# Kernel optimization log

Hardware: AMD Instinct MI355X
Metric: run time of the kernel (lower is better)

## Reference

```python
import jax, jax.numpy as jnp
import numpy as np

B, N = 64, 128
SELF_DIM, AGENT_DIM = 6, 7
C = 32            # in_mlp_dims[-1] == ia_mlp_dims[-1]
GRU_H = 2 * C     # 64
DN = ('NCHW', 'OIHW', 'NCHW')


def _lin(key, out_d, in_d):
    k1, k2 = jax.random.split(key)
    s = 1.0 / np.sqrt(in_d)
    w = jax.random.uniform(k1, (out_d, in_d), minval=-s, maxval=s, dtype=jnp.float32)
    b = jax.random.uniform(k2, (out_d,), minval=-s, maxval=s, dtype=jnp.float32)
    return w, b


def setup_inputs() -> dict:
    ks = jax.random.split(jax.random.key(0), 20)
    d = {}
    d['state'] = jax.random.normal(ks[0], (B, N, SELF_DIM + AGENT_DIM), jnp.float32)
    d['w_in1'], d['b_in1'] = _lin(ks[1], 64, AGENT_DIM)
    d['w_in2'], d['b_in2'] = _lin(ks[2], C, 64)
    s1 = 1.0 / np.sqrt(C * 9)
    d['w_c1'] = jax.random.uniform(ks[3], (64, C, 3, 3), minval=-s1, maxval=s1, dtype=jnp.float32)
    d['b_c1'] = jnp.zeros((64,), jnp.float32)
    s2 = 1.0 / np.sqrt(64 * 9)
    d['w_c2'] = jax.random.uniform(ks[4], (C, 64, 3, 3), minval=-s2, maxval=s2, dtype=jnp.float32)
    d['b_c2'] = jnp.zeros((C,), jnp.float32)
    d['w_ia1'], d['b_ia1'] = _lin(ks[5], 64, C)
    d['w_ia2'], d['b_ia2'] = _lin(ks[6], C, 64)
    d['w_s1'], d['b_s1'] = _lin(ks[7], 64, C + SELF_DIM)
    d['w_s2'], d['b_s2'] = _lin(ks[8], 32, 64)
    d['w_a1'], d['b_a1'] = _lin(ks[9], 64, 64)
    d['w_a2'], d['b_a2'] = _lin(ks[10], 32, 64)
    d['w_a3'], d['b_a3'] = _lin(ks[11], 1, 32)
    d['w_z'], _ = _lin(ks[12], GRU_H, 2 * GRU_H)
    d['w_r'], _ = _lin(ks[13], GRU_H, 2 * GRU_H)
    d['w_q'], _ = _lin(ks[14], GRU_H, 2 * GRU_H)
    d['w_m1'], d['b_m1'] = _lin(ks[15], 128, GRU_H + SELF_DIM)
    d['w_m2'], d['b_m2'] = _lin(ks[16], 64, 128)
    d['w_m3'], d['b_m3'] = _lin(ks[17], 1, 64)
    return d


def _forward(state, w_in1, b_in1, w_in2, b_in2, w_c1, b_c1, w_c2, b_c2,
             w_ia1, b_ia1, w_ia2, b_ia2, w_s1, b_s1, w_s2, b_s2,
             w_a1, b_a1, w_a2, b_a2, w_a3, b_a3, w_z, w_r, w_q,
             w_m1, b_m1, w_m2, b_m2, w_m3, b_m3):
    self_state = state[:, :, :SELF_DIM]            # (B, N, 6)
    agents = state[:, :, SELF_DIM:]                # (B, N, 7)

    # input_mlp (last_relu=True)
    h = jax.nn.relu(agents @ w_in1.T + b_in1)
    in_out = jax.nn.relu(h @ w_in2.T + b_in2)      # (B, N, C)

    # ---- AFAModule: pairwise N x N construction + conv2d edge-MLP + softmax agg ----
    f = in_out.transpose(0, 2, 1)                  # (B, C, N)
    eye = jnp.eye(N, dtype=f.dtype)
    # pair[b,c,i,j] = f[b,c,i] - f[b,c,j] + f[b,c,i]*delta_ij
    pair = f[:, :, :, None] - f[:, :, None, :] + f[:, :, :, None] * eye  # (B, C, N, N)
    w = jax.lax.conv_general_dilated(pair, w_c1, (1, 1), 'SAME', dimension_numbers=DN)
    w = jax.nn.relu(w + b_c1[None, :, None, None])
    w = jax.lax.conv_general_dilated(w, w_c2, (1, 1), 'SAME', dimension_numbers=DN)
    w = w + b_c2[None, :, None, None]
    w = jax.nn.softmax(w, axis=-1)
    afa = (pair * w).sum(-1)                        # (B, C, N)
    afa = afa.reshape(B, N, C)                      # faithful to torch .view (no transpose)
    x = in_out + afa

    # ia_mlp
    h1 = jax.nn.relu(x @ w_ia1.T + b_ia1)
    ia = h1 @ w_ia2.T + b_ia2                       # (B, N, C)

    # sort_mlp
    sort_in = jnp.concatenate([ia, self_state], axis=-1)  # (B, N, C+6)
    s1 = jax.nn.relu(sort_in @ w_s1.T + b_s1)
    sort_out = s1 @ w_s2.T + b_s2                   # (B, N, 32)
    gstate = jnp.broadcast_to(jnp.mean(sort_out, 1, keepdims=True), (B, N, 32))
    sort_mlp_input = jnp.concatenate([sort_out, gstate], axis=-1)  # (B, N, 64)

    # attention scores with masked-exp normalization
    a1 = jax.nn.relu(sort_mlp_input @ w_a1.T + b_a1)
    a2 = jax.nn.relu(a1 @ w_a2.T + b_a2)
    scores = (a2 @ w_a3.T + b_a3)[..., 0]           # (B, N)
    scores_exp = jnp.exp(scores) * (scores != 0).astype(scores.dtype)
    weights = (scores_exp / jnp.sum(scores_exp, 1, keepdims=True))[..., None]
    weighted = weights * sort_mlp_input             # (B, N, 64)

    # custom conv1d GRU (kernel 1, no bias -> channel matmuls)
    gru_input = weighted.reshape(B, GRU_H, N)       # faithful to torch .view
    h0 = sort_mlp_input.transpose(0, 2, 1)          # (B, 64, N)
    hx = jnp.concatenate([h0, gru_input], axis=1)   # (B, 128, N)
    z = jax.nn.sigmoid(jnp.einsum('oc,bcn->bon', w_z, hx))
    r = jax.nn.sigmoid(jnp.einsum('oc,bcn->bon', w_r, hx))
    q = jnp.tanh(jnp.einsum('oc,bcn->bon', w_q, jnp.concatenate([r * h0, gru_input], axis=1)))
    hn = (1 - z) * h0 + z * q
    hn = jnp.mean(hn, axis=2)                       # (B, 64)

    joint = jnp.concatenate([self_state[:, 0, :], hn], axis=1)  # (B, 70)
    m1 = jax.nn.relu(joint @ w_m1.T + b_m1)
    m2 = jax.nn.relu(m1 @ w_m2.T + b_m2)
    value = m2 @ w_m3.T + b_m3
    return value.reshape(B, -1)


def reference(state, w_in1, b_in1, w_in2, b_in2, w_c1, b_c1, w_c2, b_c2,
              w_ia1, b_ia1, w_ia2, b_ia2, w_s1, b_s1, w_s2, b_s2,
              w_a1, b_a1, w_a2, b_a2, w_a3, b_a3, w_z, w_r, w_q,
              w_m1, b_m1, w_m2, b_m2, w_m3, b_m3):
    return _forward(state, w_in1, b_in1, w_in2, b_in2, w_c1, b_c1, w_c2, b_c2,
                    w_ia1, b_ia1, w_ia2, b_ia2, w_s1, b_s1, w_s2, b_s2,
                    w_a1, b_a1, w_a2, b_a2, w_a3, b_a3, w_z, w_r, w_q,
                    w_m1, b_m1, w_m2, b_m2, w_m3, b_m3)
```

## Files before the change

kernel.cpp:

```cpp
#include <hip/hip_runtime.h>
#include <math.h>


typedef short bf16x8 __attribute__((ext_vector_type(8)));
typedef float f32x16 __attribute__((ext_vector_type(16)));

__device__ inline unsigned int bf16_rne(float x) {
  unsigned int u = __float_as_uint(x);
  return (u + 0x7fffu + ((u >> 16) & 1u)) >> 16;
}

#define MF(A, B, Cc) __builtin_amdgcn_mfma_f32_32x32x16_bf16((A), (B), (Cc), 0, 0, 0)

__global__ __launch_bounds__(256) void k0_pack(const float* __restrict__ w_c2,
                                               unsigned short* __restrict__ Apack) {
  for (int idx = threadIdx.x; idx < 36864; idx += 256) {
    int p = idx / 18432, rem = idx % 18432;
    int rx = rem >> 11, r2 = rem & 2047;
    int chunk = r2 >> 9, r3 = r2 & 511;
    int lane = r3 >> 3, i8 = r3 & 7;
    int o2 = lane & 31, k8 = lane >> 5;
    int cin = chunk * 16 + k8 * 8 + i8;
    float v = w_c2[(o2 * 64 + cin) * 9 + rx];
    unsigned int hi = bf16_rne(v);
    float hif = __uint_as_float(hi << 16);
    unsigned int lo = bf16_rne(v - hif);
    Apack[idx] = (unsigned short)(p ? lo : hi);
  }
}

__global__ __launch_bounds__(128) void k1_front(
    const float* __restrict__ state, const float* __restrict__ w_in1,
    const float* __restrict__ b_in1, const float* __restrict__ w_in2,
    const float* __restrict__ b_in2, float* __restrict__ f) {
  int b = blockIdx.x, nq = blockIdx.y, t = threadIdx.x;
  int row = t >> 2, lane = t & 3;
  int n = nq * 32 + row;
  __shared__ float hs[32][66];
  const float* st = state + (b * 128 + n) * 13 + 6;
  float a[7];
#pragma unroll
  for (int k = 0; k < 7; k++) a[k] = st[k];
  for (int oi = 0; oi < 16; oi++) {
    int o = lane * 16 + oi;
    float acc = b_in1[o];
#pragma unroll
    for (int k = 0; k < 7; k++) acc += w_in1[o * 7 + k] * a[k];
    hs[row][o] = fmaxf(acc, 0.f);
  }
  __syncthreads();
  for (int ci = 0; ci < 8; ci++) {
    int c = lane * 8 + ci;
    float acc = b_in2[c];
#pragma unroll 8
    for (int k = 0; k < 64; k++) acc += w_in2[c * 64 + k] * hs[row][k];
    f[(b * 32 + c) * 128 + n] = fmaxf(acc, 0.f);
  }
}

__global__ __launch_bounds__(128) void k2_pre(
    const float* __restrict__ f, const float* __restrict__ w_c1,
    float* __restrict__ R, float* __restrict__ C, float* __restrict__ D) {
  int o = blockIdx.x, b = blockIdx.y, t = threadIdx.x;
  __shared__ float fL[32 * 128];
  __shared__ float w1s[32 * 9];
  __shared__ float wrow[32 * 9];
  __shared__ float wcol[32 * 9];
  for (int idx = t; idx < 4096; idx += 128) fL[idx] = f[b * 4096 + idx];
  for (int idx = t; idx < 288; idx += 128) w1s[idx] = w_c1[o * 288 + idx];
  __syncthreads();
  if (t < 32) {
    int c = t;
#pragma unroll
    for (int di = 0; di < 3; di++) {
      float w0 = w1s[c * 9 + di * 3 + 0], w1 = w1s[c * 9 + di * 3 + 1],
            w2 = w1s[c * 9 + di * 3 + 2];
      wrow[(c * 3 + di) * 3 + 0] = w1 + w2;
      wrow[(c * 3 + di) * 3 + 1] = w0 + w1 + w2;
      wrow[(c * 3 + di) * 3 + 2] = w0 + w1;
    }
#pragma unroll
    for (int dj = 0; dj < 3; dj++) {
      float w0 = w1s[c * 9 + 0 * 3 + dj], w1 = w1s[c * 9 + 1 * 3 + dj],
            w2 = w1s[c * 9 + 2 * 3 + dj];
      wcol[(c * 3 + dj) * 3 + 0] = w1 + w2;
      wcol[(c * 3 + dj) * 3 + 1] = w0 + w1 + w2;
      wcol[(c * 3 + dj) * 3 + 2] = w0 + w1;
    }
  }
  __syncthreads();
  int i = t;
  float r0 = 0, r1 = 0, r2 = 0, c0 = 0, c1 = 0, c2 = 0;
  float d0 = 0, d1 = 0, d2 = 0, d3 = 0, d4 = 0;
  for (int c = 0; c < 32; c++) {
    float fm = (i >= 1) ? fL[c * 128 + i - 1] : 0.f;
    float f0 = fL[c * 128 + i];
    float fp = (i < 127) ? fL[c * 128 + i + 1] : 0.f;
    const float* wr = &wrow[c * 9];
    r0 += fm * wr[0] + f0 * wr[3] + fp * wr[6];
    r1 += fm * wr[1] + f0 * wr[4] + fp * wr[7];
    r2 += fm * wr[2] + f0 * wr[5] + fp * wr[8];
    const float* wc = &wcol[c * 9];
    c0 += fm * wc[0] + f0 * wc[3] + fp * wc[6];
    c1 += fm * wc[1] + f0 * wc[4] + fp * wc[7];
    c2 += fm * wc[2] + f0 * wc[5] + fp * wc[8];
    const float* wp = &w1s[c * 9];
    d0 += fm * wp[2];
    d1 += fm * wp[1] + f0 * wp[5];
    d2 += fm * wp[0] + f0 * wp[4] + fp * wp[8];
    d3 += f0 * wp[3] + fp * wp[7];
    d4 += fp * wp[6];
  }
  R[((b * 3 + 0) * 64 + o) * 128 + i] = r0;
  R[((b * 3 + 1) * 64 + o) * 128 + i] = r1;
  R[((b * 3 + 2) * 64 + o) * 128 + i] = r2;
  C[((b * 3 + 0) * 64 + o) * 128 + i] = c0;
  C[((b * 3 + 1) * 64 + o) * 128 + i] = c1;
  C[((b * 3 + 2) * 64 + o) * 128 + i] = c2;
  float* dp = &D[((b * 64 + o) * 128 + i) * 5];
  dp[0] = d0; dp[1] = d1; dp[2] = d2; dp[3] = d3; dp[4] = d4;
}

__global__ __launch_bounds__(256, 2) void k3_conv2(
    const float* __restrict__ f, const float* __restrict__ R,
    const float* __restrict__ C, const float* __restrict__ D,
    const float* __restrict__ b_c1, const unsigned short* __restrict__ Apack,
    const float* __restrict__ b_c2, float* __restrict__ afa) {
  extern __shared__ unsigned short G[];
  int iblk = blockIdx.x, b = blockIdx.y, t = threadIdx.x;
  int i0 = iblk * 2;
  int lane = t & 63, jt = t >> 6;
  int nn = lane & 31;
  int ccoff_half = (lane >> 5) * 8;
  const bf16x8* A8 = (const bf16x8*)Apack;
  bf16x8 zero8 = {0, 0, 0, 0, 0, 0, 0, 0};
  f32x16 acc0 = {0, 0, 0, 0, 0, 0, 0, 0, 0, 0, 0, 0, 0, 0, 0, 0};
  f32x16 acc1 = {0, 0, 0, 0, 0, 0, 0, 0, 0, 0, 0, 0, 0, 0, 0, 0};

  int ccp = t >> 2;
  int ipl = ccp >> 4;
  int cpr = ccp & 15;
  int q = t & 3;
  int j0r = q * 32;
  int ip = i0 - 1 + ipl;
  bool rowok = (ip >= 0 && ip <= 127);
  int ipc = ip < 0 ? 0 : (ip > 127 ? 127 : ip);
  int ic = (ipc == 0) ? 0 : ((ipc == 127) ? 2 : 1);

  for (int half = 0; half < 2; half++) {
    if (half) __syncthreads();
    {
      int cc = half * 32 + cpr * 2;
      float bias0 = b_c1[cc], bias1 = b_c1[cc + 1];
      float base0 = R[((b * 3 + 1) * 64 + cc) * 128 + ipc] + bias0;
      float base1 = R[((b * 3 + 1) * 64 + cc + 1) * 128 + ipc] + bias1;
      float r0v0 = 0, r0v1 = 0, r2v0 = 0, r2v1 = 0;
      if (q == 0) {
        r0v0 = R[((b * 3 + 0) * 64 + cc) * 128 + ipc] + bias0;
        r0v1 = R[((b * 3 + 0) * 64 + cc + 1) * 128 + ipc] + bias1;
      }
      if (q == 3) {
        r2v0 = R[((b * 3 + 2) * 64 + cc) * 128 + ipc] + bias0;
        r2v1 = R[((b * 3 + 2) * 64 + cc + 1) * 128 + ipc] + bias1;
      }
      const float* C0 = &C[((b * 3 + ic) * 64 + cc) * 128 + j0r];
      const float* C1 = C0 + 128;
      const float* D0 = &D[((b * 64 + cc) * 128 + ipc) * 5];
      const float* D1 = D0 + 640;
      unsigned int gbase = (unsigned)((ipl * 128 + j0r) * 40 + 2 * cpr);
#pragma unroll
      for (int s4i = 0; s4i < 8; s4i++) {
        int s4 = (s4i + q) & 7;
        float4 c0 = ((const float4*)C0)[s4];
        float4 c1 = ((const float4*)C1)[s4];
        float v0[4], v1[4];
        v0[0] = base0 - c0.x; v0[1] = base0 - c0.y;
        v0[2] = base0 - c0.z; v0[3] = base0 - c0.w;
        v1[0] = base1 - c1.x; v1[1] = base1 - c1.y;
        v1[2] = base1 - c1.z; v1[3] = base1 - c1.w;
        if (q == 0 && s4 == 0) { v0[0] = r0v0 - c0.x; v1[0] = r0v1 - c1.x; }
        if (q == 3 && s4 == 7) { v0[3] = r2v0 - c0.w; v1[3] = r2v1 - c1.w; }
#pragma unroll
        for (int t5 = 0; t5 < 5; t5++) {
          int rel = (ip - 2 + t5) - (j0r + s4 * 4);
          if (rel >= 0 && rel < 4) { v0[rel] += D0[t5]; v1[rel] += D1[t5]; }
        }
#pragma unroll
        for (int k = 0; k < 4; k++) {
          float a0 = rowok ? fmaxf(v0[k], 0.f) : 0.f;
          float a1 = rowok ? fmaxf(v1[k], 0.f) : 0.f;
          unsigned int h0 = bf16_rne(a0), h1 = bf16_rne(a1);
          float l0f = a0 - __uint_as_float(h0 << 16);
          float l1f = a1 - __uint_as_float(h1 << 16);
          unsigned int l0 = bf16_rne(l0f), l1 = bf16_rne(l1f);
          unsigned int off = gbase + (unsigned)((s4 * 4 + k) * 40);
          *(unsigned int*)&G[off] = h0 | (h1 << 16);
          *(unsigned int*)&G[off + 20480] = l0 | (l1 << 16);
        }
      }
    }
    __syncthreads();
    for (int cb = 0; cb < 2; cb++) {
      int chunk = half * 2 + cb;
      bf16x8 Ah[9], Al[9];
#pragma unroll
      for (int rx = 0; rx < 9; rx++) {
        Ah[rx] = A8[(rx * 4 + chunk) * 64 + lane];
        Al[rx] = A8[((9 + rx) * 4 + chunk) * 64 + lane];
      }
      int ccoff = cb * 16 + ccoff_half;
#pragma unroll
      for (int rowidx = 0; rowidx < 4; rowidx++) {
#pragma unroll
        for (int x = 0; x < 3; x++) {
          int imgj = jt * 32 + nn + x - 1;
          int ij = imgj < 0 ? 0 : (imgj > 127 ? 127 : imgj);
          int off = (rowidx * 128 + ij) * 40 + ccoff;
          bf16x8 bh = *(const bf16x8*)&G[off];
          bf16x8 bl = *(const bf16x8*)&G[off + 20480];
          if (imgj < 0 || imgj > 127) { bh = zero8; bl = zero8; }
          if (rowidx == 0) {
            acc0 = MF(Ah[x], bh, acc0);
            acc0 = MF(Ah[x], bl, acc0);
            acc0 = MF(Al[x], bh, acc0);
          } else if (rowidx == 1) {
            acc0 = MF(Ah[3 + x], bh, acc0);
            acc0 = MF(Ah[3 + x], bl, acc0);
            acc0 = MF(Al[3 + x], bh, acc0);
            acc1 = MF(Ah[x], bh, acc1);
            acc1 = MF(Ah[x], bl, acc1);
            acc1 = MF(Al[x], bh, acc1);
          } else if (rowidx == 2) {
            acc0 = MF(Ah[6 + x], bh, acc0);
            acc0 = MF(Ah[6 + x], bl, acc0);
            acc0 = MF(Al[6 + x], bh, acc0);
            acc1 = MF(Ah[3 + x], bh, acc1);
            acc1 = MF(Ah[3 + x], bl, acc1);
            acc1 = MF(Al[3 + x], bh, acc1);
          } else {
            acc1 = MF(Ah[6 + x], bh, acc1);
            acc1 = MF(Ah[6 + x], bl, acc1);
            acc1 = MF(Al[6 + x], bh, acc1);
          }
        }
      }
    }
  }
  __syncthreads();
  const int LSTR = 129;
  float* logits = (float*)G;
  float* fbuf = (float*)G + 64 * LSTR;
#pragma unroll
  for (int reg = 0; reg < 16; reg++) {
    int o2 = (reg & 3) + 8 * (reg >> 2) + 4 * (lane >> 5);
    int j = jt * 32 + nn;
    logits[(0 * 32 + o2) * LSTR + j] = acc0[reg];
    logits[(1 * 32 + o2) * LSTR + j] = acc1[reg];
  }
  for (int idx = t; idx < 1024; idx += 256) {
    float4 v = ((const float4*)(f + b * 4096))[idx];
    int c = idx >> 5, s4 = idx & 31;
    float* dst = &fbuf[c * LSTR + s4 * 4];
    dst[0] = v.x; dst[1] = v.y; dst[2] = v.z; dst[3] = v.w;
  }
  __syncthreads();
  {
    int i2 = t >> 7, o2e = (t >> 2) & 31, qd = t & 3;
    int rot = qd * 8;
    const float* lrow = &logits[(i2 * 32 + o2e) * LSTR + qd * 32];
    float bias2 = b_c2[o2e];
    float vals[32];
    float mx = -3.0e38f;
#pragma unroll
    for (int s = 0; s < 32; s++) {
      vals[s] = lrow[(s + rot) & 31] + bias2;
      mx = fmaxf(mx, vals[s]);
    }
    mx = fmaxf(mx, __shfl_xor(mx, 1));
    mx = fmaxf(mx, __shfl_xor(mx, 2));
    float sum = 0.f;
#pragma unroll
    for (int s = 0; s < 32; s++) {
      vals[s] = expf(vals[s] - mx);
      sum += vals[s];
    }
    sum += __shfl_xor(sum, 1);
    sum += __shfl_xor(sum, 2);
    float inv = 1.f / sum;
    int gi = i0 + i2;
    float fi = fbuf[o2e * LSTR + gi];
    float part = 0.f;
#pragma unroll
    for (int s = 0; s < 32; s++) {
      int j = qd * 32 + ((s + rot) & 31);
      float w = vals[s] * inv;
      part += w * (fi - fbuf[o2e * LSTR + j]);
      if (j == gi) part += w * fi;
    }
    part += __shfl_xor(part, 1);
    part += __shfl_xor(part, 2);
    if (qd == 0) afa[(b * 32 + o2e) * 128 + gi] = part;
  }
}

__global__ __launch_bounds__(256) void k4a_sort(
    const float* __restrict__ state, const float* __restrict__ f,
    const float* __restrict__ afa, const float* __restrict__ w_ia1,
    const float* __restrict__ b_ia1, const float* __restrict__ w_ia2,
    const float* __restrict__ b_ia2, const float* __restrict__ w_s1,
    const float* __restrict__ b_s1, const float* __restrict__ w_s2,
    const float* __restrict__ b_s2, float* __restrict__ so_g) {
  int blk = blockIdx.x;
  int b = blk >> 2, nq = blk & 3;
  int t = threadIdx.x, row = t >> 3, lane = t & 7;
  int n = nq * 32 + row;
  __shared__ float bufA[32][40];
  __shared__ float bufB[32][72];
  {
    int c0 = lane * 4;
    float4 av = *(const float4*)&afa[b * 4096 + n * 32 + c0];
    bufA[row][c0 + 0] = f[b * 4096 + (c0 + 0) * 128 + n] + av.x;
    bufA[row][c0 + 1] = f[b * 4096 + (c0 + 1) * 128 + n] + av.y;
    bufA[row][c0 + 2] = f[b * 4096 + (c0 + 2) * 128 + n] + av.z;
    bufA[row][c0 + 3] = f[b * 4096 + (c0 + 3) * 128 + n] + av.w;
  }
  __syncthreads();
#pragma unroll
  for (int oi = 0; oi < 8; oi++) {
    int o = lane * 8 + oi;
    float a = b_ia1[o];
#pragma unroll 8
    for (int c = 0; c < 32; c++) a += w_ia1[o * 32 + c] * bufA[row][c];
    bufB[row][o] = fmaxf(a, 0.f);
  }
  __syncthreads();
  {
    float r0[4];
#pragma unroll
    for (int oi = 0; oi < 4; oi++) {
      int o = lane * 4 + oi;
      float a = b_ia2[o];
#pragma unroll 8
      for (int k = 0; k < 64; k++) a += w_ia2[o * 64 + k] * bufB[row][k];
      r0[oi] = a;
    }
    __syncthreads();
#pragma unroll
    for (int oi = 0; oi < 4; oi++) bufA[row][lane * 4 + oi] = r0[oi];
    if (lane == 0) {
#pragma unroll
      for (int k = 0; k < 6; k++)
        bufA[row][32 + k] = state[(b * 128 + n) * 13 + k];
    }
  }
  __syncthreads();
#pragma unroll
  for (int oi = 0; oi < 8; oi++) {
    int o = lane * 8 + oi;
    float a = b_s1[o];
#pragma unroll 2
    for (int k = 0; k < 38; k++) a += w_s1[o * 38 + k] * bufA[row][k];
    bufB[row][o] = fmaxf(a, 0.f);
  }
  __syncthreads();
#pragma unroll
  for (int oi = 0; oi < 4; oi++) {
    int o = lane * 4 + oi;
    float a = b_s2[o];
#pragma unroll 8
    for (int k = 0; k < 64; k++) a += w_s2[o * 64 + k] * bufB[row][k];
    so_g[(b * 128 + n) * 32 + o] = a;
  }
}

__global__ __launch_bounds__(128) void k4b_gstate(const float* __restrict__ so_g,
                                                  float* __restrict__ gst) {
  int b = blockIdx.x, t = threadIdx.x;
  int c = t & 31, part = t >> 5;
  __shared__ float red[4][32];
  float a = 0.f;
  for (int nn = 0; nn < 32; nn++) a += so_g[(b * 128 + part * 32 + nn) * 32 + c];
  red[part][c] = a;
  __syncthreads();
  if (t < 32) gst[b * 32 + t] =
      (red[0][t] + red[1][t] + red[2][t] + red[3][t]) * (1.f / 128.f);
}

__global__ __launch_bounds__(256) void k4c_attn(
    const float* __restrict__ so_g, const float* __restrict__ gst,
    const float* __restrict__ w_a1, const float* __restrict__ b_a1,
    const float* __restrict__ w_a2, const float* __restrict__ b_a2,
    const float* __restrict__ w_a3, const float* __restrict__ b_a3,
    float* __restrict__ smi, float* __restrict__ se_g) {
  int blk = blockIdx.x;
  int b = blk >> 2, nq = blk & 3;
  int t = threadIdx.x, row = t >> 3, lane = t & 7;
  int n = nq * 32 + row;
  __shared__ float bufA[32][72];
  __shared__ float bufB[32][72];
  {
    int c0 = lane * 4;
    float4 sv = *(const float4*)&so_g[(b * 128 + n) * 32 + c0];
    float4 gv = *(const float4*)&gst[b * 32 + c0];
    *(float4*)&bufA[row][c0] = sv;
    *(float4*)&bufA[row][32 + c0] = gv;
    *(float4*)&smi[b * 8192 + n * 64 + c0] = sv;
    *(float4*)&smi[b * 8192 + n * 64 + 32 + c0] = gv;
  }
  __syncthreads();
#pragma unroll
  for (int oi = 0; oi < 8; oi++) {
    int o = lane * 8 + oi;
    float a = b_a1[o];
#pragma unroll 8
    for (int k = 0; k < 64; k++) a += w_a1[o * 64 + k] * bufA[row][k];
    bufB[row][o] = fmaxf(a, 0.f);
  }
  __syncthreads();
  float ps = 0.f;
#pragma unroll
  for (int oi = 0; oi < 4; oi++) {
    int o = lane * 4 + oi;
    float a = b_a2[o];
#pragma unroll 8
    for (int k = 0; k < 64; k++) a += w_a2[o * 64 + k] * bufB[row][k];
    ps += w_a3[o] * fmaxf(a, 0.f);
  }
  for (int d = 4; d >= 1; d >>= 1) ps += __shfl_xor(ps, d, 8);
  if (lane == 0) {
    float sc = ps + b_a3[0];
    se_g[b * 128 + n] = (sc != 0.f) ? expf(sc) : 0.f;
  }
}

__global__ __launch_bounds__(128) void k4d_wts(const float* __restrict__ se_g,
                                               float* __restrict__ wts) {
  int b = blockIdx.x, n = threadIdx.x;
  __shared__ float red[128];
  float se = se_g[b * 128 + n];
  red[n] = se;
  __syncthreads();
  for (int s = 64; s >= 1; s >>= 1) {
    if (n < s) red[n] += red[n + s];
    __syncthreads();
  }
  wts[b * 128 + n] = se / red[0];
}

__global__ __launch_bounds__(256) void k5a_r(
    const float* __restrict__ smi, const float* __restrict__ wts,
    const float* __restrict__ w_r, float* __restrict__ rh) {
  int cch = blockIdx.x, b = blockIdx.y, t = threadIdx.x;
  __shared__ float smi_s[128 * 65];
  __shared__ float wts_s[128];
  for (int idx = t; idx < 8192; idx += 256) {
    int n = idx >> 6, k = idx & 63;
    smi_s[n * 65 + k] = smi[b * 8192 + idx];
  }
  if (t < 128) wts_s[t] = wts[b * 128 + t];
  __syncthreads();
  int c = cch * 16 + (t >> 4), l = t & 15;
  float accs[8];
#pragma unroll
  for (int m = 0; m < 8; m++) accs[m] = 0.f;
  const float* wr = &w_r[c * 128];
  for (int k = 0; k < 64; k++) {
    float wv = wr[k];
#pragma unroll
    for (int m = 0; m < 8; m++) accs[m] += wv * smi_s[(l + 16 * m) * 65 + k];
  }
  for (int c2 = 0; c2 < 64; c2++) {
    float wv = wr[64 + c2];
    float g0 = wts_s[2 * c2], g1 = wts_s[2 * c2 + 1];
#pragma unroll
    for (int m = 0; m < 8; m++) {
      int nb = (m >> 2) & 1, nl = l + 16 * (m & 3);
      accs[m] += wv * ((nb ? g1 : g0) * smi_s[(2 * c2 + nb) * 65 + nl]);
    }
  }
#pragma unroll
  for (int m = 0; m < 8; m++) {
    int n = l + 16 * m;
    float r = 1.f / (1.f + expf(-accs[m]));
    rh[(b * 64 + c) * 128 + n] = r * smi_s[n * 65 + c];
  }
}

__global__ __launch_bounds__(256) void k5b_gru(
    const float* __restrict__ smi, const float* __restrict__ wts,
    const float* __restrict__ rh, const float* __restrict__ w_z,
    const float* __restrict__ w_q, float* __restrict__ hnm) {
  int och = blockIdx.x, b = blockIdx.y, t = threadIdx.x;
  __shared__ float smi_s[128 * 65];
  __shared__ float wts_s[128];
  for (int idx = t; idx < 8192; idx += 256) {
    int n = idx >> 6, k = idx & 63;
    smi_s[n * 65 + k] = smi[b * 8192 + idx];
  }
  if (t < 128) wts_s[t] = wts[b * 128 + t];
  __syncthreads();
  int o = och * 16 + (t >> 4), l = t & 15;
  float az[8], aq[8];
#pragma unroll
  for (int m = 0; m < 8; m++) { az[m] = 0.f; aq[m] = 0.f; }
  const float* wz = &w_z[o * 128];
  const float* wq = &w_q[o * 128];
  const float* rhb = rh + b * 8192;
  for (int k = 0; k < 64; k++) {
    float wv = wz[k];
#pragma unroll
    for (int m = 0; m < 8; m++) az[m] += wv * smi_s[(l + 16 * m) * 65 + k];
  }
  for (int c = 0; c < 64; c++) {
    float wv = wq[c];
#pragma unroll
    for (int m = 0; m < 8; m++) aq[m] += wv * rhb[c * 128 + l + 16 * m];
  }
  for (int c2 = 0; c2 < 64; c2++) {
    float wvz = wz[64 + c2], wvq = wq[64 + c2];
    float g0 = wts_s[2 * c2], g1 = wts_s[2 * c2 + 1];
#pragma unroll
    for (int m = 0; m < 8; m++) {
      int nb = (m >> 2) & 1, nl = l + 16 * (m & 3);
      float gin = (nb ? g1 : g0) * smi_s[(2 * c2 + nb) * 65 + nl];
      az[m] += wvz * gin;
      aq[m] += wvq * gin;
    }
  }
  float part = 0.f;
#pragma unroll
  for (int m = 0; m < 8; m++) {
    int n = l + 16 * m;
    float z = 1.f / (1.f + expf(-az[m]));
    float q = tanhf(aq[m]);
    float h0 = smi_s[n * 65 + o];
    part += (1.f - z) * h0 + z * q;
  }
  for (int d = 8; d >= 1; d >>= 1) part += __shfl_xor(part, d, 16);
  if (l == 0) hnm[b * 64 + o] = part * (1.f / 128.f);
}

__global__ __launch_bounds__(128, 1) void k6_head(
    const float* __restrict__ state, const float* __restrict__ hnm,
    const float* __restrict__ w_m1, const float* __restrict__ b_m1,
    const float* __restrict__ w_m2, const float* __restrict__ b_m2,
    const float* __restrict__ w_m3, const float* __restrict__ b_m3,
    float* __restrict__ out) {
  int b = blockIdx.x, t = threadIdx.x;
  __shared__ float joint[70];
  __shared__ float m1s[128];
  __shared__ float red[64];
  if (t < 6) joint[t] = state[b * 1664 + t];
  if (t < 64) joint[6 + t] = hnm[b * 64 + t];
  __syncthreads();
  float a = b_m1[t];
#pragma unroll 2
  for (int k = 0; k < 70; k++) a += w_m1[t * 70 + k] * joint[k];
  m1s[t] = fmaxf(a, 0.f);
  __syncthreads();
  if (t < 64) {
    float a2 = b_m2[t];
#pragma unroll 8
    for (int k = 0; k < 128; k++) a2 += w_m2[t * 128 + k] * m1s[k];
    red[t] = fmaxf(a2, 0.f) * w_m3[t];
  }
  __syncthreads();
  for (int s = 32; s >= 1; s >>= 1) {
    if (t < s) red[t] += red[t + s];
    __syncthreads();
  }
  if (t == 0) out[b] = red[0] + b_m3[0];
}

extern "C" void kernel_launch(void* const* d_in, const int* in_sizes, int n_in,
                              void* d_out, int out_size, void* d_ws, size_t ws_size,
                              hipStream_t stream) {
  const float* state = (const float*)d_in[0];
  const float* w_in1 = (const float*)d_in[1];
  const float* b_in1 = (const float*)d_in[2];
  const float* w_in2 = (const float*)d_in[3];
  const float* b_in2 = (const float*)d_in[4];
  const float* w_c1  = (const float*)d_in[5];
  const float* b_c1  = (const float*)d_in[6];
  const float* w_c2  = (const float*)d_in[7];
  const float* b_c2  = (const float*)d_in[8];
  const float* w_ia1 = (const float*)d_in[9];
  const float* b_ia1 = (const float*)d_in[10];
  const float* w_ia2 = (const float*)d_in[11];
  const float* b_ia2 = (const float*)d_in[12];
  const float* w_s1  = (const float*)d_in[13];
  const float* b_s1  = (const float*)d_in[14];
  const float* w_s2  = (const float*)d_in[15];
  const float* b_s2  = (const float*)d_in[16];
  const float* w_a1  = (const float*)d_in[17];
  const float* b_a1  = (const float*)d_in[18];
  const float* w_a2  = (const float*)d_in[19];
  const float* b_a2  = (const float*)d_in[20];
  const float* w_a3  = (const float*)d_in[21];
  const float* b_a3  = (const float*)d_in[22];
  const float* w_z   = (const float*)d_in[23];
  const float* w_r   = (const float*)d_in[24];
  const float* w_q   = (const float*)d_in[25];
  const float* w_m1  = (const float*)d_in[26];
  const float* b_m1  = (const float*)d_in[27];
  const float* w_m2  = (const float*)d_in[28];
  const float* b_m2  = (const float*)d_in[29];
  const float* w_m3  = (const float*)d_in[30];
  const float* b_m3  = (const float*)d_in[31];
  float* ws    = (float*)d_ws;
  float* f_    = ws;
  float* R_    = ws + 262144;
  float* C_    = ws + 1835008;
  float* D_    = ws + 3407872;
  float* afa_  = ws + 6029312;
  float* smi_  = ws + 6291456;
  float* wts_  = ws + 6815744;
  float* rh_   = ws + 6823936;
  float* hnm_  = ws + 7348224;
  unsigned short* Apack_ = (unsigned short*)(ws + 7352320);
  float* so_   = ws + 7376896;
  float* gst_  = ws + 7639040;
  float* se_   = ws + 7641088;
  float* out   = (float*)d_out;

  k0_pack<<<1, 256, 0, stream>>>(w_c2, Apack_);
  k1_front<<<dim3(64, 4), 128, 0, stream>>>(state, w_in1, b_in1, w_in2, b_in2, f_);
  k2_pre<<<dim3(64, 64), 128, 0, stream>>>(f_, w_c1, R_, C_, D_);
  k3_conv2<<<dim3(64, 64), 256, 81920, stream>>>(f_, R_, C_, D_, b_c1, Apack_,
                                                 b_c2, afa_);
  k4a_sort<<<256, 256, 0, stream>>>(state, f_, afa_, w_ia1, b_ia1, w_ia2, b_ia2,
                                    w_s1, b_s1, w_s2, b_s2, so_);
  k4b_gstate<<<64, 128, 0, stream>>>(so_, gst_);
  k4c_attn<<<256, 256, 0, stream>>>(so_, gst_, w_a1, b_a1, w_a2, b_a2, w_a3,
                                    b_a3, smi_, se_);
  k4d_wts<<<64, 128, 0, stream>>>(se_, wts_);
  k5a_r<<<dim3(4, 64), 256, 0, stream>>>(smi_, wts_, w_r, rh_);
  k5b_gru<<<dim3(4, 64), 256, 0, stream>>>(smi_, wts_, rh_, w_z, w_q, hnm_);
  k6_head<<<64, 128, 0, stream>>>(state, hnm_, w_m1, b_m1, w_m2, b_m2, w_m3,
                                  b_m3, out);
}
```

Baseline: 483.0 us.

## Fuse small kernels, double conv2 block to 512 threads, use packed bf16 convert

Folds the weight-pack kernel into k1_front as an extra grid row, folds the global-state mean into k4c_attn, and folds the weight normalization into k5a/k5b, removing three small launches and their round trips through global memory. k3_conv2 now runs 512 threads per block, splitting the channel chunks across two wave groups whose partial logits are summed through shared memory, and the softmax stage uses 8 lanes per row. The bf16 hi/lo split uses the v_cvt_pk_bf16_f32 instruction instead of manual rounding. In exchange, the GRU kernels repeat the normalization reduction in every block, and k3 adds an extra barrier plus a shared-memory accumulate pass.

```diff
diff --git a/kernel.cpp b/kernel.cpp
--- a/kernel.cpp
+++ b/kernel.cpp
@@ -10,30 +10,37 @@
   return (u + 0x7fffu + ((u >> 16) & 1u)) >> 16;
 }
 
+__device__ inline unsigned int pk_bf16(float a, float b) {
+  unsigned int r;
+  asm("v_cvt_pk_bf16_f32 %0, %1, %2" : "=v"(r) : "v"(a), "v"(b));
+  return r;
+}
+
 #define MF(A, B, Cc) __builtin_amdgcn_mfma_f32_32x32x16_bf16((A), (B), (Cc), 0, 0, 0)
-
-__global__ __launch_bounds__(256) void k0_pack(const float* __restrict__ w_c2,
-                                               unsigned short* __restrict__ Apack) {
-  for (int idx = threadIdx.x; idx < 36864; idx += 256) {
-    int p = idx / 18432, rem = idx % 18432;
-    int rx = rem >> 11, r2 = rem & 2047;
-    int chunk = r2 >> 9, r3 = r2 & 511;
-    int lane = r3 >> 3, i8 = r3 & 7;
-    int o2 = lane & 31, k8 = lane >> 5;
-    int cin = chunk * 16 + k8 * 8 + i8;
-    float v = w_c2[(o2 * 64 + cin) * 9 + rx];
-    unsigned int hi = bf16_rne(v);
-    float hif = __uint_as_float(hi << 16);
-    unsigned int lo = bf16_rne(v - hif);
-    Apack[idx] = (unsigned short)(p ? lo : hi);
-  }
-}
 
 __global__ __launch_bounds__(128) void k1_front(
     const float* __restrict__ state, const float* __restrict__ w_in1,
     const float* __restrict__ b_in1, const float* __restrict__ w_in2,
-    const float* __restrict__ b_in2, float* __restrict__ f) {
+    const float* __restrict__ b_in2, float* __restrict__ f,
+    const float* __restrict__ w_c2, unsigned short* __restrict__ Apack) {
   int b = blockIdx.x, nq = blockIdx.y, t = threadIdx.x;
+  if (nq == 4) {
+    int base = b * 576;
+    for (int idx = base + t; idx < base + 576; idx += 128) {
+      int p = idx / 18432, rem = idx % 18432;
+      int rx = rem >> 11, r2 = rem & 2047;
+      int chunk = r2 >> 9, r3 = r2 & 511;
+      int lane = r3 >> 3, i8 = r3 & 7;
+      int o2 = lane & 31, k8 = lane >> 5;
+      int cin = chunk * 16 + k8 * 8 + i8;
+      float v = w_c2[(o2 * 64 + cin) * 9 + rx];
+      unsigned int hi = bf16_rne(v);
+      float hif = __uint_as_float(hi << 16);
+      unsigned int lo = bf16_rne(v - hif);
+      Apack[idx] = (unsigned short)(p ? lo : hi);
+    }
+    return;
+  }
   int row = t >> 2, lane = t & 3;
   int n = nq * 32 + row;
   __shared__ float hs[32][66];
@@ -121,7 +128,7 @@
   dp[0] = d0; dp[1] = d1; dp[2] = d2; dp[3] = d3; dp[4] = d4;
 }
 
-__global__ __launch_bounds__(256, 2) void k3_conv2(
+__global__ __launch_bounds__(512, 4) void k3_conv2(
     const float* __restrict__ f, const float* __restrict__ R,
     const float* __restrict__ C, const float* __restrict__ D,
     const float* __restrict__ b_c1, const unsigned short* __restrict__ Apack,
@@ -129,7 +136,8 @@
   extern __shared__ unsigned short G[];
   int iblk = blockIdx.x, b = blockIdx.y, t = threadIdx.x;
   int i0 = iblk * 2;
-  int lane = t & 63, jt = t >> 6;
+  int lane = t & 63, wv = t >> 6;
+  int jt = wv & 3, cg = wv >> 2;
   int nn = lane & 31;
   int ccoff_half = (lane >> 5) * 8;
   const bf16x8* A8 = (const bf16x8*)Apack;
@@ -137,9 +145,9 @@
   f32x16 acc0 = {0, 0, 0, 0, 0, 0, 0, 0, 0, 0, 0, 0, 0, 0, 0, 0};
   f32x16 acc1 = {0, 0, 0, 0, 0, 0, 0, 0, 0, 0, 0, 0, 0, 0, 0, 0};
 
-  int ccp = t >> 2;
-  int ipl = ccp >> 4;
-  int cpr = ccp & 15;
+  int ipl = t >> 7;
+  int sh = (t >> 6) & 1;
+  int cpr = (t >> 2) & 15;
   int q = t & 3;
   int j0r = q * 32;
   int ip = i0 - 1 + ipl;
@@ -155,11 +163,11 @@
       float base0 = R[((b * 3 + 1) * 64 + cc) * 128 + ipc] + bias0;
       float base1 = R[((b * 3 + 1) * 64 + cc + 1) * 128 + ipc] + bias1;
       float r0v0 = 0, r0v1 = 0, r2v0 = 0, r2v1 = 0;
-      if (q == 0) {
+      if (q == 0 && sh == 0) {
         r0v0 = R[((b * 3 + 0) * 64 + cc) * 128 + ipc] + bias0;
         r0v1 = R[((b * 3 + 0) * 64 + cc + 1) * 128 + ipc] + bias1;
       }
-      if (q == 3) {
+      if (q == 3 && sh == 1) {
         r2v0 = R[((b * 3 + 2) * 64 + cc) * 128 + ipc] + bias0;
         r2v1 = R[((b * 3 + 2) * 64 + cc + 1) * 128 + ipc] + bias1;
       }
@@ -169,8 +177,8 @@
       const float* D1 = D0 + 640;
       unsigned int gbase = (unsigned)((ipl * 128 + j0r) * 40 + 2 * cpr);
 #pragma unroll
-      for (int s4i = 0; s4i < 8; s4i++) {
-        int s4 = (s4i + q) & 7;
+      for (int u = 0; u < 4; u++) {
+        int s4 = (sh * 4 + u + q) & 7;
         float4 c0 = ((const float4*)C0)[s4];
         float4 c1 = ((const float4*)C1)[s4];
         float v0[4], v1[4];
@@ -189,26 +197,26 @@
         for (int k = 0; k < 4; k++) {
           float a0 = rowok ? fmaxf(v0[k], 0.f) : 0.f;
           float a1 = rowok ? fmaxf(v1[k], 0.f) : 0.f;
-          unsigned int h0 = bf16_rne(a0), h1 = bf16_rne(a1);
-          float l0f = a0 - __uint_as_float(h0 << 16);
-          float l1f = a1 - __uint_as_float(h1 << 16);
-          unsigned int l0 = bf16_rne(l0f), l1 = bf16_rne(l1f);
+          unsigned int hw = pk_bf16(a0, a1);
+          float h0f = __uint_as_float(hw << 16);
+          float h1f = __uint_as_float(hw & 0xffff0000u);
+          unsigned int lw = pk_bf16(a0 - h0f, a1 - h1f);
           unsigned int off = gbase + (unsigned)((s4 * 4 + k) * 40);
-          *(unsigned int*)&G[off] = h0 | (h1 << 16);
-          *(unsigned int*)&G[off + 20480] = l0 | (l1 << 16);
+          *(unsigned int*)&G[off] = hw;
+          *(unsigned int*)&G[off + 20480] = lw;
         }
       }
     }
     __syncthreads();
-    for (int cb = 0; cb < 2; cb++) {
-      int chunk = half * 2 + cb;
+    {
+      int chunk = half * 2 + cg;
       bf16x8 Ah[9], Al[9];
 #pragma unroll
       for (int rx = 0; rx < 9; rx++) {
         Ah[rx] = A8[(rx * 4 + chunk) * 64 + lane];
         Al[rx] = A8[((9 + rx) * 4 + chunk) * 64 + lane];
       }
-      int ccoff = cb * 16 + ccoff_half;
+      int ccoff = cg * 16 + ccoff_half;
 #pragma unroll
       for (int rowidx = 0; rowidx < 4; rowidx++) {
 #pragma unroll
@@ -250,56 +258,73 @@
   const int LSTR = 129;
   float* logits = (float*)G;
   float* fbuf = (float*)G + 64 * LSTR;
-#pragma unroll
-  for (int reg = 0; reg < 16; reg++) {
-    int o2 = (reg & 3) + 8 * (reg >> 2) + 4 * (lane >> 5);
-    int j = jt * 32 + nn;
-    logits[(0 * 32 + o2) * LSTR + j] = acc0[reg];
-    logits[(1 * 32 + o2) * LSTR + j] = acc1[reg];
-  }
-  for (int idx = t; idx < 1024; idx += 256) {
-    float4 v = ((const float4*)(f + b * 4096))[idx];
-    int c = idx >> 5, s4 = idx & 31;
-    float* dst = &fbuf[c * LSTR + s4 * 4];
-    dst[0] = v.x; dst[1] = v.y; dst[2] = v.z; dst[3] = v.w;
+  int j = jt * 32 + nn;
+  if (cg == 0) {
+#pragma unroll
+    for (int reg = 0; reg < 16; reg++) {
+      int o2 = (reg & 3) + 8 * (reg >> 2) + 4 * (lane >> 5);
+      logits[(0 * 32 + o2) * LSTR + j] = acc0[reg];
+      logits[(1 * 32 + o2) * LSTR + j] = acc1[reg];
+    }
+  } else {
+    for (int idx = t - 256; idx < 1024; idx += 256) {
+      float4 v = ((const float4*)(f + b * 4096))[idx];
+      int c = idx >> 5, s4f = idx & 31;
+      float* dst = &fbuf[c * LSTR + s4f * 4];
+      dst[0] = v.x; dst[1] = v.y; dst[2] = v.z; dst[3] = v.w;
+    }
+  }
+  __syncthreads();
+  if (cg == 1) {
+#pragma unroll
+    for (int reg = 0; reg < 16; reg++) {
+      int o2 = (reg & 3) + 8 * (reg >> 2) + 4 * (lane >> 5);
+      logits[(0 * 32 + o2) * LSTR + j] += acc0[reg];
+      logits[(1 * 32 + o2) * LSTR + j] += acc1[reg];
+    }
   }
   __syncthreads();
   {
-    int i2 = t >> 7, o2e = (t >> 2) & 31, qd = t & 3;
-    int rot = qd * 8;
-    const float* lrow = &logits[(i2 * 32 + o2e) * LSTR + qd * 32];
+    int i2 = t >> 8;
+    int o2e = (t >> 3) & 31;
+    int qe = t & 7;
+    int rot = (qe * 2) & 15;
+    const float* lrow = &logits[(i2 * 32 + o2e) * LSTR + qe * 16];
     float bias2 = b_c2[o2e];
-    float vals[32];
+    float vals[16];
     float mx = -3.0e38f;
 #pragma unroll
-    for (int s = 0; s < 32; s++) {
-      vals[s] = lrow[(s + rot) & 31] + bias2;
+    for (int s = 0; s < 16; s++) {
+      vals[s] = lrow[(s + rot) & 15] + bias2;
       mx = fmaxf(mx, vals[s]);
     }
     mx = fmaxf(mx, __shfl_xor(mx, 1));
     mx = fmaxf(mx, __shfl_xor(mx, 2));
+    mx = fmaxf(mx, __shfl_xor(mx, 4));
     float sum = 0.f;
 #pragma unroll
-    for (int s = 0; s < 32; s++) {
+    for (int s = 0; s < 16; s++) {
       vals[s] = expf(vals[s] - mx);
       sum += vals[s];
     }
     sum += __shfl_xor(sum, 1);
     sum += __shfl_xor(sum, 2);
+    sum += __shfl_xor(sum, 4);
     float inv = 1.f / sum;
     int gi = i0 + i2;
     float fi = fbuf[o2e * LSTR + gi];
     float part = 0.f;
 #pragma unroll
-    for (int s = 0; s < 32; s++) {
-      int j = qd * 32 + ((s + rot) & 31);
+    for (int s = 0; s < 16; s++) {
+      int jj = qe * 16 + ((s + rot) & 15);
       float w = vals[s] * inv;
-      part += w * (fi - fbuf[o2e * LSTR + j]);
-      if (j == gi) part += w * fi;
+      part += w * (fi - fbuf[o2e * LSTR + jj]);
+      if (jj == gi) part += w * fi;
     }
     part += __shfl_xor(part, 1);
     part += __shfl_xor(part, 2);
-    if (qd == 0) afa[(b * 32 + o2e) * 128 + gi] = part;
+    part += __shfl_xor(part, 4);
+    if (qe == 0) afa[(b * 32 + o2e) * 128 + gi] = part;
   }
 }
 
@@ -373,38 +398,45 @@
   }
 }
 
-__global__ __launch_bounds__(128) void k4b_gstate(const float* __restrict__ so_g,
-                                                  float* __restrict__ gst) {
-  int b = blockIdx.x, t = threadIdx.x;
-  int c = t & 31, part = t >> 5;
-  __shared__ float red[4][32];
-  float a = 0.f;
-  for (int nn = 0; nn < 32; nn++) a += so_g[(b * 128 + part * 32 + nn) * 32 + c];
-  red[part][c] = a;
-  __syncthreads();
-  if (t < 32) gst[b * 32 + t] =
-      (red[0][t] + red[1][t] + red[2][t] + red[3][t]) * (1.f / 128.f);
-}
-
 __global__ __launch_bounds__(256) void k4c_attn(
-    const float* __restrict__ so_g, const float* __restrict__ gst,
-    const float* __restrict__ w_a1, const float* __restrict__ b_a1,
-    const float* __restrict__ w_a2, const float* __restrict__ b_a2,
-    const float* __restrict__ w_a3, const float* __restrict__ b_a3,
-    float* __restrict__ smi, float* __restrict__ se_g) {
+    const float* __restrict__ so_g, const float* __restrict__ w_a1,
+    const float* __restrict__ b_a1, const float* __restrict__ w_a2,
+    const float* __restrict__ b_a2, const float* __restrict__ w_a3,
+    const float* __restrict__ b_a3, float* __restrict__ smi,
+    float* __restrict__ se_g) {
   int blk = blockIdx.x;
   int b = blk >> 2, nq = blk & 3;
   int t = threadIdx.x, row = t >> 3, lane = t & 7;
   int n = nq * 32 + row;
   __shared__ float bufA[32][72];
   __shared__ float bufB[32][72];
+  __shared__ float gred[8][32];
+  __shared__ float gs_s[32];
+  {
+    int c = t & 31, grp = t >> 5;
+    float s = 0.f;
+#pragma unroll 4
+    for (int k = 0; k < 16; k++) s += so_g[(b * 128 + grp * 16 + k) * 32 + c];
+    gred[grp][c] = s;
+  }
   {
     int c0 = lane * 4;
     float4 sv = *(const float4*)&so_g[(b * 128 + n) * 32 + c0];
-    float4 gv = *(const float4*)&gst[b * 32 + c0];
     *(float4*)&bufA[row][c0] = sv;
+    *(float4*)&smi[b * 8192 + n * 64 + c0] = sv;
+  }
+  __syncthreads();
+  if (t < 32) {
+    float s = 0.f;
+#pragma unroll
+    for (int g = 0; g < 8; g++) s += gred[g][t];
+    gs_s[t] = s * (1.f / 128.f);
+  }
+  __syncthreads();
+  {
+    int c0 = lane * 4;
+    float4 gv = *(const float4*)&gs_s[c0];
     *(float4*)&bufA[row][32 + c0] = gv;
-    *(float4*)&smi[b * 8192 + n * 64 + c0] = sv;
     *(float4*)&smi[b * 8192 + n * 64 + 32 + c0] = gv;
   }
   __syncthreads();
@@ -433,31 +465,26 @@
   }
 }
 
-__global__ __launch_bounds__(128) void k4d_wts(const float* __restrict__ se_g,
-                                               float* __restrict__ wts) {
-  int b = blockIdx.x, n = threadIdx.x;
-  __shared__ float red[128];
-  float se = se_g[b * 128 + n];
-  red[n] = se;
-  __syncthreads();
-  for (int s = 64; s >= 1; s >>= 1) {
-    if (n < s) red[n] += red[n + s];
-    __syncthreads();
-  }
-  wts[b * 128 + n] = se / red[0];
-}
-
 __global__ __launch_bounds__(256) void k5a_r(
-    const float* __restrict__ smi, const float* __restrict__ wts,
+    const float* __restrict__ smi, const float* __restrict__ se_g,
     const float* __restrict__ w_r, float* __restrict__ rh) {
   int cch = blockIdx.x, b = blockIdx.y, t = threadIdx.x;
   __shared__ float smi_s[128 * 65];
   __shared__ float wts_s[128];
+  __shared__ float invs_s;
   for (int idx = t; idx < 8192; idx += 256) {
     int n = idx >> 6, k = idx & 63;
     smi_s[n * 65 + k] = smi[b * 8192 + idx];
   }
-  if (t < 128) wts_s[t] = wts[b * 128 + t];
+  if (t < 128) wts_s[t] = se_g[b * 128 + t];
+  __syncthreads();
+  if (t < 64) {
+    float s2 = wts_s[t] + wts_s[t + 64];
+    for (int d = 32; d >= 1; d >>= 1) s2 += __shfl_xor(s2, d);
+    if (t == 0) invs_s = 1.f / s2;
+  }
+  __syncthreads();
+  if (t < 128) wts_s[t] *= invs_s;
   __syncthreads();
   int c = cch * 16 + (t >> 4), l = t & 15;
   float accs[8];
@@ -487,17 +514,26 @@
 }
 
 __global__ __launch_bounds__(256) void k5b_gru(
-    const float* __restrict__ smi, const float* __restrict__ wts,
+    const float* __restrict__ smi, const float* __restrict__ se_g,
     const float* __restrict__ rh, const float* __restrict__ w_z,
     const float* __restrict__ w_q, float* __restrict__ hnm) {
   int och = blockIdx.x, b = blockIdx.y, t = threadIdx.x;
   __shared__ float smi_s[128 * 65];
   __shared__ float wts_s[128];
+  __shared__ float invs_s;
   for (int idx = t; idx < 8192; idx += 256) {
     int n = idx >> 6, k = idx & 63;
     smi_s[n * 65 + k] = smi[b * 8192 + idx];
   }
-  if (t < 128) wts_s[t] = wts[b * 128 + t];
+  if (t < 128) wts_s[t] = se_g[b * 128 + t];
+  __syncthreads();
+  if (t < 64) {
+    float s2 = wts_s[t] + wts_s[t + 64];
+    for (int d = 32; d >= 1; d >>= 1) s2 += __shfl_xor(s2, d);
+    if (t == 0) invs_s = 1.f / s2;
+  }
+  __syncthreads();
+  if (t < 128) wts_s[t] *= invs_s;
   __syncthreads();
   int o = och * 16 + (t >> 4), l = t & 15;
   float az[8], aq[8];
@@ -614,28 +650,24 @@
   float* D_    = ws + 3407872;
   float* afa_  = ws + 6029312;
   float* smi_  = ws + 6291456;
-  float* wts_  = ws + 6815744;
   float* rh_   = ws + 6823936;
   float* hnm_  = ws + 7348224;
   unsigned short* Apack_ = (unsigned short*)(ws + 7352320);
   float* so_   = ws + 7376896;
-  float* gst_  = ws + 7639040;
   float* se_   = ws + 7641088;
   float* out   = (float*)d_out;
 
-  k0_pack<<<1, 256, 0, stream>>>(w_c2, Apack_);
-  k1_front<<<dim3(64, 4), 128, 0, stream>>>(state, w_in1, b_in1, w_in2, b_in2, f_);
+  k1_front<<<dim3(64, 5), 128, 0, stream>>>(state, w_in1, b_in1, w_in2, b_in2,
+                                            f_, w_c2, Apack_);
   k2_pre<<<dim3(64, 64), 128, 0, stream>>>(f_, w_c1, R_, C_, D_);
-  k3_conv2<<<dim3(64, 64), 256, 81920, stream>>>(f_, R_, C_, D_, b_c1, Apack_,
+  k3_conv2<<<dim3(64, 64), 512, 81920, stream>>>(f_, R_, C_, D_, b_c1, Apack_,
                                                  b_c2, afa_);
   k4a_sort<<<256, 256, 0, stream>>>(state, f_, afa_, w_ia1, b_ia1, w_ia2, b_ia2,
                                     w_s1, b_s1, w_s2, b_s2, so_);
-  k4b_gstate<<<64, 128, 0, stream>>>(so_, gst_);
-  k4c_attn<<<256, 256, 0, stream>>>(so_, gst_, w_a1, b_a1, w_a2, b_a2, w_a3,
-                                    b_a3, smi_, se_);
-  k4d_wts<<<64, 128, 0, stream>>>(se_, wts_);
-  k5a_r<<<dim3(4, 64), 256, 0, stream>>>(smi_, wts_, w_r, rh_);
-  k5b_gru<<<dim3(4, 64), 256, 0, stream>>>(smi_, wts_, rh_, w_z, w_q, hnm_);
+  k4c_attn<<<256, 256, 0, stream>>>(so_, w_a1, b_a1, w_a2, b_a2, w_a3, b_a3,
+                                    smi_, se_);
+  k5a_r<<<dim3(4, 64), 256, 0, stream>>>(smi_, se_, w_r, rh_);
+  k5b_gru<<<dim3(4, 64), 256, 0, stream>>>(smi_, se_, rh_, w_z, w_q, hnm_);
   k6_head<<<64, 128, 0, stream>>>(state, hnm_, w_m1, b_m1, w_m2, b_m2, w_m3,
                                   b_m3, out);
 }
```

Result: faster. 447.3 us (-7.4%).
